# Optimization experiments

Hardware: AMD Instinct MI355X
Metric: run time of the kernel (lower is better)

Reference implementation:

```python
import jax, jax.numpy as jnp
import numpy as np


def _conv(x, w, b=None, stride=1, pad=0):
    y = jax.lax.conv_general_dilated(x, w, (stride, stride), [(pad, pad), (pad, pad)],
                                     dimension_numbers=('NCHW', 'OIHW', 'NCHW'))
    if b is not None:
        y = y + b[None, :, None, None]
    return y


def _slice3d(grid, guide):
    # Trilinear grid_sample, align_corners=False, zero padding.
    # grid: (N, C=12, D=8, GH, GW); guide: (N,1,H,W) in [-1,1]
    N, C, D, GH, GW = grid.shape
    H, W = guide.shape[2], guide.shape[3]
    xs = 2.0 * jnp.arange(W, dtype=grid.dtype) / max(W - 1, 1) - 1.0
    ys = 2.0 * jnp.arange(H, dtype=grid.dtype) / max(H - 1, 1) - 1.0
    gx = ((xs + 1.0) * GW - 1.0) * 0.5               # (W,)
    gy = ((ys + 1.0) * GH - 1.0) * 0.5               # (H,)
    gz = ((guide[:, 0] + 1.0) * D - 1.0) * 0.5       # (N,H,W)
    x0f = jnp.floor(gx); y0f = jnp.floor(gy); z0f = jnp.floor(gz)
    fx = gx - x0f; fy = gy - y0f; fz = gz - z0f
    x0 = x0f.astype(jnp.int32); y0 = y0f.astype(jnp.int32); z0 = z0f.astype(jnp.int32)
    gf = grid.reshape(N, C, D * GH * GW)

    def corner(zi, yi, xi, wz, wy, wx):
        mask = ((zi >= 0) & (zi < D)) & ((yi >= 0) & (yi < GH))[None, :, None] & ((xi >= 0) & (xi < GW))[None, None, :]
        zc = jnp.clip(zi, 0, D - 1); yc = jnp.clip(yi, 0, GH - 1); xc = jnp.clip(xi, 0, GW - 1)
        flat = zc * (GH * GW) + yc[None, :, None] * GW + xc[None, None, :]   # (N,H,W)
        v = jnp.take_along_axis(gf, flat.reshape(N, 1, H * W), axis=2).reshape(N, C, H, W)
        w = (wz * wy[None, :, None] * wx[None, None, :]) * mask.astype(grid.dtype)  # (N,H,W)
        return v * w[:, None]

    out = jnp.zeros((N, C, H, W), grid.dtype)
    for dz in (0, 1):
        for dy in (0, 1):
            for dx in (0, 1):
                out = out + corner(z0 + dz, y0 + dy, x0 + dx,
                                   fz if dz else 1.0 - fz,
                                   fy if dy else 1.0 - fy,
                                   fx if dx else 1.0 - fx)
    return out


def setup_inputs() -> dict:
    key = jax.random.key(0)
    ks = jax.random.split(key, 40)
    def w(i, shape):
        return jax.random.normal(ks[i], shape, jnp.float32) * 0.05
    return {
        'low_res': jax.random.uniform(ks[0], (4, 3, 256, 256), jnp.float32),
        'full_res': jax.random.uniform(ks[1], (4, 1, 1024, 1024), jnp.float32),
        'w0': w(2, (8, 3, 3, 3)), 'b0': w(3, (8,)),
        'w1': w(4, (16, 8, 3, 3)), 'b1': w(5, (16,)),
        'w2': w(6, (32, 16, 3, 3)), 'b2': w(7, (32,)),
        'w3': w(8, (64, 32, 3, 3)), 'b3': w(9, (64,)),
        'wl0': w(10, (64, 64, 3, 3)), 'bl0': w(11, (64,)),
        'wl1': w(12, (64, 64, 3, 3)),
        'wg1': w(13, (128, 64, 3, 3)), 'bg1': w(14, (128,)),
        'wg2': w(15, (256, 128, 3, 3)), 'bg2': w(16, (256,)),
        'wf1': w(17, (256, 448, 1, 1)), 'bf1': w(18, (256,)),
        'wf2': w(19, (128, 256, 1, 1)), 'bf2': w(20, (128,)),
        'wf3': w(21, (64, 128, 1, 1)), 'bf3': w(22, (64,)),
        'wlin': w(23, (96, 64, 1, 1)), 'blin': w(24, (96,)),
        'wgd1': w(25, (16, 1, 3, 3)), 'bgd1': w(26, (16,)),
        'wgd2': w(27, (1, 16, 1, 1)), 'bgd2': w(28, (1,)),
        'wau1': w(29, (16, 1, 1, 1)), 'bau1': w(30, (16,)),
        'wau2': w(31, (1, 16, 1, 1)), 'bau2': w(32, (1,)),
        'wav1': w(33, (16, 1, 1, 1)), 'bav1': w(34, (16,)),
        'wav2': w(35, (1, 16, 1, 1)), 'bav2': w(36, (1,)),
    }


def reference(low_res, full_res, w0, b0, w1, b1, w2, b2, w3, b3, wl0, bl0, wl1,
              wg1, bg1, wg2, bg2, wf1, bf1, wf2, bf2, wf3, bf3, wlin, blin,
              wgd1, bgd1, wgd2, bgd2, wau1, bau1, wau2, bau2, wav1, bav1, wav2, bav2):
    relu = jax.nn.relu
    N = low_res.shape[0]
    H, W = full_res.shape[2], full_res.shape[3]
    fake = jax.image.resize(low_res, (N, 3, H, W), 'bilinear')
    # splat stack: 4 stride-2 convs
    x = relu(_conv(low_res, w0, b0, 2, 1))
    x = relu(_conv(x, w1, b1, 2, 1))
    x = relu(_conv(x, w2, b2, 2, 1))
    splat = relu(_conv(x, w3, b3, 2, 1))                 # (N,64,16,16)
    local = _conv(relu(_conv(splat, wl0, bl0, 1, 1)), wl1, None, 1, 1)
    # global branch
    a0 = splat.mean(axis=(2, 3), keepdims=True)
    x1 = relu(_conv(splat, wg1, bg1, 2, 1))
    a1 = x1.mean(axis=(2, 3), keepdims=True)
    x2 = relu(_conv(x1, wg2, bg2, 2, 1))
    a2 = x2.mean(axis=(2, 3), keepdims=True)
    a = jnp.concatenate([a0, a1, a2], axis=1)            # (N,448,1,1)
    a = relu(_conv(a, wf1, bf1))
    a = relu(_conv(a, wf2, bf2))
    glob = relu(_conv(a, wf3, bf3))                      # (N,64,1,1)
    fused = relu(glob + local)
    fused = _conv(fused, wlin, blin)                     # (N,96,16,16)
    grid = fused.reshape(N, 12, 8, fused.shape[2], fused.shape[3])
    guidemap = jnp.tanh(_conv(relu(_conv(full_res, wgd1, bgd1, 1, 1)), wgd2, bgd2))
    coeff = _slice3d(grid, guidemap)                     # (N,12,H,W)
    Y = full_res * coeff[:, 3:4] + coeff[:, 0:3].sum(axis=1, keepdims=True)
    U0 = full_res * coeff[:, 7:8] + coeff[:, 4:7].sum(axis=1, keepdims=True)
    V0 = full_res * coeff[:, 11:12] + coeff[:, 8:11].sum(axis=1, keepdims=True)
    U = jnp.tanh(_conv(relu(_conv(U0, wau1, bau1)), wau2, bau2)) + fake[:, 1:2]
    V = jnp.tanh(_conv(relu(_conv(V0, wav1, bav1)), wav2, bav2)) + fake[:, 2:3]
    return jnp.concatenate([Y, U, V], axis=1)
```

## Files before the change

kernel.cpp:

```cpp
#include <hip/hip_runtime.h>
#include <math.h>


__device__ __forceinline__ float tanh_fast(float x) {
    float e = __expf(2.0f * x);
    return 1.0f - 2.0f / (e + 1.0f);
}

template<int CIN, int COUT, int HIN, int WIN, int HOUT, int WOUT>
__global__ __launch_bounds__(256) void conv_s2_small(
    const float* __restrict__ in, const float* __restrict__ w,
    const float* __restrict__ b, float* __restrict__ out)
{
    int idx = blockIdx.x * 256 + threadIdx.x;
    int wo = idx % WOUT; int t = idx / WOUT;
    int ho = t % HOUT; t /= HOUT;
    int co = t % COUT; int n = t / COUT;
    float acc = b[co];
    int hi0 = ho * 2 - 1, wi0 = wo * 2 - 1;
    const float* wp = w + (size_t)co * CIN * 9;
    #pragma unroll
    for (int ci = 0; ci < CIN; ++ci) {
        const float* ip = in + ((size_t)(n * CIN + ci)) * HIN * WIN;
        const float* wc = wp + ci * 9;
        #pragma unroll
        for (int kh = 0; kh < 3; ++kh) {
            int hi = hi0 + kh;
            if ((unsigned)hi >= (unsigned)HIN) continue;
            const float* row = ip + hi * WIN;
            #pragma unroll
            for (int kw = 0; kw < 3; ++kw) {
                int wi = wi0 + kw;
                if ((unsigned)wi >= (unsigned)WIN) continue;
                acc = fmaf(wc[kh * 3 + kw], row[wi], acc);
            }
        }
    }
    out[idx] = fmaxf(acc, 0.0f);
}

template<int CIN, int PARTS, int STRIDE, bool RELU, bool HASB,
         int COUT, int HIN, int WIN, int HOUT, int WOUT>
__device__ __forceinline__ void conv_p_dev(
    const float* __restrict__ in, const float* __restrict__ w,
    const float* __restrict__ b, float* __restrict__ out,
    int tb, float* red)
{
    constexpr int CPT = CIN / PARTS;
    constexpr int OPB = 256 / PARTS;
    int part = threadIdx.x / OPB;
    int oidx = threadIdx.x % OPB;
    int o = tb * OPB + oidx;
    int wo = o % WOUT; int t = o / WOUT;
    int ho = t % HOUT; t /= HOUT;
    int co = t % COUT; int n = t / COUT;
    int hi0 = ho * STRIDE - 1, wi0 = wo * STRIDE - 1;
    const float* wp = w + ((size_t)co * CIN + part * CPT) * 9;
    const float* ip = in + ((size_t)n * CIN + part * CPT) * HIN * WIN;
    float acc = 0.0f;
    #pragma unroll
    for (int ci = 0; ci < CPT; ++ci) {
        const float* ic = ip + (size_t)ci * HIN * WIN;
        const float* wc = wp + ci * 9;
        #pragma unroll
        for (int kh = 0; kh < 3; ++kh) {
            int hi = hi0 + kh;
            if ((unsigned)hi >= (unsigned)HIN) continue;
            const float* row = ic + hi * WIN;
            #pragma unroll
            for (int kw = 0; kw < 3; ++kw) {
                int wi = wi0 + kw;
                if ((unsigned)wi >= (unsigned)WIN) continue;
                acc = fmaf(wc[kh * 3 + kw], row[wi], acc);
            }
        }
    }
    red[threadIdx.x] = acc;
    __syncthreads();
    if (part == 0) {
        float s = acc;
        #pragma unroll
        for (int p = 1; p < PARTS; ++p) s += red[p * OPB + oidx];
        if (HASB) s += b[co];
        if (RELU) s = fmaxf(s, 0.0f);
        out[o] = s;
    }
}

__global__ __launch_bounds__(256) void conv2_k(
    const float* __restrict__ in, const float* __restrict__ w,
    const float* __restrict__ b, float* __restrict__ out)
{
    __shared__ float red[256];
    conv_p_dev<16, 4, 2, true, true, 32, 64, 64, 32, 32>(in, w, b, out, blockIdx.x, red);
}

__global__ __launch_bounds__(256) void conv3_k(
    const float* __restrict__ in, const float* __restrict__ w,
    const float* __restrict__ b, float* __restrict__ out)
{
    __shared__ float red[256];
    conv_p_dev<32, 8, 2, true, true, 64, 32, 32, 16, 16>(in, w, b, out, blockIdx.x, red);
}

__global__ __launch_bounds__(256) void k5_l0_g1_means(
    const float* __restrict__ splat,
    const float* __restrict__ wl0, const float* __restrict__ bl0, float* __restrict__ l0o,
    const float* __restrict__ wg1, const float* __restrict__ bg1, float* __restrict__ x1,
    float* __restrict__ avec)
{
    __shared__ float red[256];
    int bid = blockIdx.x;
    if (bid < 4096) {
        conv_p_dev<64, 16, 1, true, true, 64, 16, 16, 16, 16>(splat, wl0, bl0, l0o, bid, red);
    } else if (bid < 6144) {
        conv_p_dev<64, 16, 2, true, true, 128, 16, 16, 8, 8>(splat, wg1, bg1, x1, bid - 4096, red);
    } else {
        int wid = (bid - 6144) * 4 + (threadIdx.x >> 6);
        int lane = threadIdx.x & 63;
        int n = wid >> 6, c = wid & 63;
        const float* p = splat + ((size_t)(n * 64 + c)) * 256;
        float s = p[lane] + p[lane + 64] + p[lane + 128] + p[lane + 192];
        #pragma unroll
        for (int off = 32; off; off >>= 1) s += __shfl_down(s, off, 64);
        if (lane == 0) avec[n * 448 + c] = s * (1.0f / 256.0f);
    }
}

__global__ __launch_bounds__(256) void k6_l1_g2_means(
    const float* __restrict__ l0o, const float* __restrict__ wl1, float* __restrict__ localb,
    const float* __restrict__ x1, const float* __restrict__ wg2,
    const float* __restrict__ bg2, float* __restrict__ x2,
    float* __restrict__ avec)
{
    __shared__ float red[256];
    int bid = blockIdx.x;
    if (bid < 4096) {
        conv_p_dev<64, 16, 1, false, false, 64, 16, 16, 16, 16>(l0o, wl1, nullptr, localb, bid, red);
    } else if (bid < 5120) {
        conv_p_dev<128, 16, 2, true, true, 256, 8, 8, 4, 4>(x1, wg2, bg2, x2, bid - 4096, red);
    } else {
        int wid = (bid - 5120) * 4 + (threadIdx.x >> 6);
        int lane = threadIdx.x & 63;
        int n = wid >> 7, c = wid & 127;
        const float* p = x1 + ((size_t)(n * 128 + c)) * 64;
        float s = p[lane];
        #pragma unroll
        for (int off = 32; off; off >>= 1) s += __shfl_down(s, off, 64);
        if (lane == 0) avec[n * 448 + 64 + c] = s * (1.0f / 64.0f);
    }
}

__global__ __launch_bounds__(256) void kfc_fuse(
    const float* __restrict__ avec, const float* __restrict__ x2,
    const float* __restrict__ wf1, const float* __restrict__ bf1,
    const float* __restrict__ wf2, const float* __restrict__ bf2,
    const float* __restrict__ wf3, const float* __restrict__ bf3,
    const float* __restrict__ local,
    const float* __restrict__ wlin, const float* __restrict__ blin,
    float* __restrict__ grid)
{
    __shared__ float a[448];
    __shared__ float h1[256];
    __shared__ float h2[128];
    __shared__ float gl[64];
    int n = blockIdx.x / 96; int k = blockIdx.x % 96; int t = threadIdx.x;
    if (t < 192) a[t] = avec[n * 448 + t];
    {
        const float* p = x2 + ((size_t)(n * 256 + t)) * 16;
        float s = 0.0f;
        #pragma unroll
        for (int i = 0; i < 16; ++i) s += p[i];
        a[192 + t] = s * (1.0f / 16.0f);
    }
    __syncthreads();
    {
        float a0 = 0, a1 = 0, a2 = 0, a3 = 0;
        const float* wp = wf1 + (size_t)t * 448;
        for (int i = 0; i < 448; i += 4) {
            a0 = fmaf(wp[i], a[i], a0); a1 = fmaf(wp[i + 1], a[i + 1], a1);
            a2 = fmaf(wp[i + 2], a[i + 2], a2); a3 = fmaf(wp[i + 3], a[i + 3], a3);
        }
        h1[t] = fmaxf(a0 + a1 + a2 + a3 + bf1[t], 0.0f);
    }
    __syncthreads();
    if (t < 128) {
        float a0 = 0, a1 = 0, a2 = 0, a3 = 0;
        const float* wp = wf2 + (size_t)t * 256;
        for (int i = 0; i < 256; i += 4) {
            a0 = fmaf(wp[i], h1[i], a0); a1 = fmaf(wp[i + 1], h1[i + 1], a1);
            a2 = fmaf(wp[i + 2], h1[i + 2], a2); a3 = fmaf(wp[i + 3], h1[i + 3], a3);
        }
        h2[t] = fmaxf(a0 + a1 + a2 + a3 + bf2[t], 0.0f);
    }
    __syncthreads();
    if (t < 64) {
        float a0 = 0, a1 = 0, a2 = 0, a3 = 0;
        const float* wp = wf3 + (size_t)t * 128;
        for (int i = 0; i < 128; i += 4) {
            a0 = fmaf(wp[i], h2[i], a0); a1 = fmaf(wp[i + 1], h2[i + 1], a1);
            a2 = fmaf(wp[i + 2], h2[i + 2], a2); a3 = fmaf(wp[i + 3], h2[i + 3], a3);
        }
        gl[t] = fmaxf(a0 + a1 + a2 + a3 + bf3[t], 0.0f);
    }
    __syncthreads();
    float acc = blin[k];
    const float* wp = wlin + k * 64;
    const float* lo = local + (size_t)n * 64 * 256 + t;
    #pragma unroll 8
    for (int c = 0; c < 64; ++c)
        acc = fmaf(wp[c], fmaxf(gl[c] + lo[c * 256], 0.0f), acc);
    int ch = k >> 3; int z = k & 7;
    grid[(((size_t)(n * 8 + z)) * 256 + t) * 12 + ch] = acc;
}

__global__ __launch_bounds__(256) void hdr_out_v2(
    const float* __restrict__ full, const float* __restrict__ low,
    const float* __restrict__ grid,
    const float* __restrict__ wgd1, const float* __restrict__ bgd1,
    const float* __restrict__ wgd2, const float* __restrict__ bgd2,
    const float* __restrict__ wau1, const float* __restrict__ bau1,
    const float* __restrict__ wau2, const float* __restrict__ bau2,
    const float* __restrict__ wav1, const float* __restrict__ bav1,
    const float* __restrict__ wav2, const float* __restrict__ bav2,
    float* __restrict__ out)
{
    int tid = blockIdx.x * 256 + threadIdx.x;
    int x0 = (tid & 255) << 2;
    int y = (tid >> 8) & 1023;
    int n = tid >> 18;
    const float* fp = full + ((size_t)n << 20);

    float v[3][6];
    #pragma unroll
    for (int r = 0; r < 3; ++r) {
        int yy = y + r - 1;
        bool okr = (unsigned)yy < 1024u;
        const float* row = fp + (size_t)yy * 1024;
        if (okr) {
            float4 m = *(const float4*)(row + x0);
            v[r][1] = m.x; v[r][2] = m.y; v[r][3] = m.z; v[r][4] = m.w;
            v[r][0] = (x0 > 0) ? row[x0 - 1] : 0.0f;
            v[r][5] = (x0 < 1020) ? row[x0 + 4] : 0.0f;
        } else {
            #pragma unroll
            for (int j = 0; j < 6; ++j) v[r][j] = 0.0f;
        }
    }

    float gacc[4];
    float bb = bgd2[0];
    #pragma unroll
    for (int px = 0; px < 4; ++px) gacc[px] = bb;
    #pragma unroll
    for (int k = 0; k < 16; ++k) {
        const float* wk = wgd1 + k * 9;
        float q0 = wk[0], q1 = wk[1], q2 = wk[2];
        float q3 = wk[3], q4 = wk[4], q5 = wk[5];
        float q6 = wk[6], q7 = wk[7], q8 = wk[8];
        float bk = bgd1[k], wo = wgd2[k];
        #pragma unroll
        for (int px = 0; px < 4; ++px) {
            float h = bk;
            h = fmaf(q0, v[0][px], h); h = fmaf(q1, v[0][px + 1], h); h = fmaf(q2, v[0][px + 2], h);
            h = fmaf(q3, v[1][px], h); h = fmaf(q4, v[1][px + 1], h); h = fmaf(q5, v[1][px + 2], h);
            h = fmaf(q6, v[2][px], h); h = fmaf(q7, v[2][px + 1], h); h = fmaf(q8, v[2][px + 2], h);
            gacc[px] = fmaf(wo, fmaxf(h, 0.0f), gacc[px]);
        }
    }

    const float* gbase = grid + (size_t)n * 24576;
    float Yo[4], Uo[4], Vo[4];

    #pragma unroll
    for (int px = 0; px < 4; ++px) {
        int x = x0 + px;
        float g = tanh_fast(gacc[px]);

        float gxc = (x * (32.0f / 1023.0f) - 1.0f) * 0.5f;
        float gyc = (y * (32.0f / 1023.0f) - 1.0f) * 0.5f;
        float gzc = 4.0f * g + 3.5f;
        float x0f = floorf(gxc), y0f = floorf(gyc), z0f = floorf(gzc);
        float fx = gxc - x0f, fy = gyc - y0f, fz = gzc - z0f;
        int ix = (int)x0f, iy = (int)y0f, iz = (int)z0f;

        float wx0 = (ix >= 0 && ix < 16) ? (1.0f - fx) : 0.0f;
        float wx1 = (ix + 1 < 16) ? fx : 0.0f;
        float wy0 = (iy >= 0 && iy < 16) ? (1.0f - fy) : 0.0f;
        float wy1 = (iy + 1 < 16) ? fy : 0.0f;
        float wz0 = (iz >= 0 && iz < 8) ? (1.0f - fz) : 0.0f;
        float wz1 = (iz + 1 >= 0 && iz + 1 < 8) ? fz : 0.0f;
        int xi0 = min(max(ix, 0), 15), xi1 = min(ix + 1, 15);
        int yi0 = min(max(iy, 0), 15), yi1 = min(iy + 1, 15);
        int zi0 = min(max(iz, 0), 7),  zi1 = min(max(iz + 1, 0), 7);

        float w00 = wy0 * wx0, w01 = wy0 * wx1, w10 = wy1 * wx0, w11 = wy1 * wx1;
        int o00 = yi0 * 16 + xi0, o01 = yi0 * 16 + xi1;
        int o10 = yi1 * 16 + xi0, o11 = yi1 * 16 + xi1;
        int z0b = zi0 * 256, z1b = zi1 * 256;

        float acc[12];
        #pragma unroll
        for (int i = 0; i < 12; ++i) acc[i] = 0.0f;

        #define CORNER(OFF, WK) { \
            const float4* q = (const float4*)(gbase + (size_t)(OFF) * 12); \
            float wk_ = (WK); \
            float4 A = q[0], B = q[1], C = q[2]; \
            acc[0] = fmaf(wk_, A.x, acc[0]); acc[1] = fmaf(wk_, A.y, acc[1]); \
            acc[2] = fmaf(wk_, A.z, acc[2]); acc[3] = fmaf(wk_, A.w, acc[3]); \
            acc[4] = fmaf(wk_, B.x, acc[4]); acc[5] = fmaf(wk_, B.y, acc[5]); \
            acc[6] = fmaf(wk_, B.z, acc[6]); acc[7] = fmaf(wk_, B.w, acc[7]); \
            acc[8] = fmaf(wk_, C.x, acc[8]); acc[9] = fmaf(wk_, C.y, acc[9]); \
            acc[10] = fmaf(wk_, C.z, acc[10]); acc[11] = fmaf(wk_, C.w, acc[11]); }

        CORNER(z0b + o00, wz0 * w00)
        CORNER(z0b + o01, wz0 * w01)
        CORNER(z0b + o10, wz0 * w10)
        CORNER(z0b + o11, wz0 * w11)
        CORNER(z1b + o00, wz1 * w00)
        CORNER(z1b + o01, wz1 * w01)
        CORNER(z1b + o10, wz1 * w10)
        CORNER(z1b + o11, wz1 * w11)
        #undef CORNER

        float p = v[1][px + 1];
        float Yv = fmaf(p, acc[3],  acc[0] + acc[1] + acc[2]);
        float U0 = fmaf(p, acc[7],  acc[4] + acc[5] + acc[6]);
        float V0 = fmaf(p, acc[11], acc[8] + acc[9] + acc[10]);

        float uacc = bau2[0];
        #pragma unroll
        for (int k = 0; k < 16; ++k)
            uacc = fmaf(wau2[k], fmaxf(fmaf(wau1[k], U0, bau1[k]), 0.0f), uacc);
        float vacc = bav2[0];
        #pragma unroll
        for (int k = 0; k < 16; ++k)
            vacc = fmaf(wav2[k], fmaxf(fmaf(wav1[k], V0, bav1[k]), 0.0f), vacc);

        float sx = (x + 0.5f) * 0.25f - 0.5f;
        float sy = (y + 0.5f) * 0.25f - 0.5f;
        float sxf = floorf(sx), syf = floorf(sy);
        float fxl = sx - sxf, fyl = sy - syf;
        int jx0 = max((int)sxf, 0), jx1 = min((int)sxf + 1, 255);
        int jy0 = max((int)syf, 0), jy1 = min((int)syf + 1, 255);
        const float* lr1 = low + ((size_t)(n * 3 + 1)) * 65536;
        const float* lr2 = low + ((size_t)(n * 3 + 2)) * 65536;
        float f1 = (1.0f - fyl) * ((1.0f - fxl) * lr1[jy0 * 256 + jx0] + fxl * lr1[jy0 * 256 + jx1])
                 + fyl * ((1.0f - fxl) * lr1[jy1 * 256 + jx0] + fxl * lr1[jy1 * 256 + jx1]);
        float f2 = (1.0f - fyl) * ((1.0f - fxl) * lr2[jy0 * 256 + jx0] + fxl * lr2[jy0 * 256 + jx1])
                 + fyl * ((1.0f - fxl) * lr2[jy1 * 256 + jx0] + fxl * lr2[jy1 * 256 + jx1]);

        Yo[px] = Yv;
        Uo[px] = tanh_fast(uacc) + f1;
        Vo[px] = tanh_fast(vacc) + f2;
    }

    size_t base = ((size_t)n * 3) * 1048576 + (size_t)y * 1024 + x0;
    *(float4*)(out + base)            = make_float4(Yo[0], Yo[1], Yo[2], Yo[3]);
    *(float4*)(out + base + 1048576)  = make_float4(Uo[0], Uo[1], Uo[2], Uo[3]);
    *(float4*)(out + base + 2097152)  = make_float4(Vo[0], Vo[1], Vo[2], Vo[3]);
}

extern "C" void kernel_launch(void* const* d_in, const int* in_sizes, int n_in,
                              void* d_out, int out_size, void* d_ws, size_t ws_size,
                              hipStream_t stream)
{
    const float* low  = (const float*)d_in[0];
    const float* full = (const float*)d_in[1];
    const float* w0 = (const float*)d_in[2];  const float* b0 = (const float*)d_in[3];
    const float* w1 = (const float*)d_in[4];  const float* b1 = (const float*)d_in[5];
    const float* w2 = (const float*)d_in[6];  const float* b2 = (const float*)d_in[7];
    const float* w3 = (const float*)d_in[8];  const float* b3 = (const float*)d_in[9];
    const float* wl0 = (const float*)d_in[10]; const float* bl0 = (const float*)d_in[11];
    const float* wl1 = (const float*)d_in[12];
    const float* wg1 = (const float*)d_in[13]; const float* bg1 = (const float*)d_in[14];
    const float* wg2 = (const float*)d_in[15]; const float* bg2 = (const float*)d_in[16];
    const float* wf1 = (const float*)d_in[17]; const float* bf1 = (const float*)d_in[18];
    const float* wf2 = (const float*)d_in[19]; const float* bf2 = (const float*)d_in[20];
    const float* wf3 = (const float*)d_in[21]; const float* bf3 = (const float*)d_in[22];
    const float* wlin = (const float*)d_in[23]; const float* blin = (const float*)d_in[24];
    const float* wgd1 = (const float*)d_in[25]; const float* bgd1 = (const float*)d_in[26];
    const float* wgd2 = (const float*)d_in[27]; const float* bgd2 = (const float*)d_in[28];
    const float* wau1 = (const float*)d_in[29]; const float* bau1 = (const float*)d_in[30];
    const float* wau2 = (const float*)d_in[31]; const float* bau2 = (const float*)d_in[32];
    const float* wav1 = (const float*)d_in[33]; const float* bav1 = (const float*)d_in[34];
    const float* wav2 = (const float*)d_in[35]; const float* bav2 = (const float*)d_in[36];
    float* out = (float*)d_out;

    float* ws = (float*)d_ws;
    float* t0b    = ws;
    float* t1b    = t0b + 524288;
    float* t2b    = t1b + 262144;
    float* splat  = t2b + 131072;
    float* l0o    = splat + 65536;
    float* localb = l0o + 65536;
    float* x1b    = localb + 65536;
    float* x2b    = x1b + 32768;
    float* avec   = x2b + 16384;
    float* gridb  = avec + 1792;

    conv_s2_small<3, 8, 256, 256, 128, 128><<<2048, 256, 0, stream>>>(low, w0, b0, t0b);
    conv_s2_small<8, 16, 128, 128, 64, 64><<<1024, 256, 0, stream>>>(t0b, w1, b1, t1b);
    conv2_k<<<2048, 256, 0, stream>>>(t1b, w2, b2, t2b);
    conv3_k<<<2048, 256, 0, stream>>>(t2b, w3, b3, splat);
    k5_l0_g1_means<<<6208, 256, 0, stream>>>(splat, wl0, bl0, l0o, wg1, bg1, x1b, avec);
    k6_l1_g2_means<<<5248, 256, 0, stream>>>(l0o, wl1, localb, x1b, wg2, bg2, x2b, avec);
    kfc_fuse<<<384, 256, 0, stream>>>(avec, x2b, wf1, bf1, wf2, bf2, wf3, bf3,
                                      localb, wlin, blin, gridb);
    hdr_out_v2<<<4096, 256, 0, stream>>>(full, low, gridb,
        wgd1, bgd1, wgd2, bgd2, wau1, bau1, wau2, bau2, wav1, bav1, wav2, bav2, out);
}
```

Measured before the change: 362.7 us.

## Fuse all stages into one persistent kernel with hierarchical grid barriers

Replaces eight separate kernel launches with a single persistent kernel of 512 blocks. The blocks loop over each stage's work and synchronize through a two-level atomic grid barrier in workspace, which is cleared with a memset before launch. The aim is to remove launch overhead and the gaps between the many small early stages. In exchange, the large final per-pixel stage now runs on a fixed grid of 512 blocks with grid-stride loops. The barrier relies on all blocks being co-resident and includes a spin guard that could silently break ordering if it expires.

```diff
diff --git a/kernel.cpp b/kernel.cpp
--- a/kernel.cpp
+++ b/kernel.cpp
@@ -1,18 +1,45 @@
 #include <hip/hip_runtime.h>
 #include <math.h>
 
+
+#define NBLK 512
+#define NTHR 256
+#define GSZ (NBLK * NTHR)
 
 __device__ __forceinline__ float tanh_fast(float x) {
     float e = __expf(2.0f * x);
     return 1.0f - 2.0f / (e + 1.0f);
 }
 
+__device__ __forceinline__ void gsync(int* bar, int id) {
+    __syncthreads();
+    if (threadIdx.x == 0) {
+        int* base = bar + id * 1088;
+        int* grp  = base + ((blockIdx.x >> 4) << 5);
+        int* root = base + 1024;
+        int* flag = base + 1056;
+        __threadfence();
+        if (atomicAdd(grp, 1) == 15) {
+            if (atomicAdd(root, 1) == 31) {
+                __threadfence();
+                __hip_atomic_store(flag, 1, __ATOMIC_RELEASE, __HIP_MEMORY_SCOPE_AGENT);
+            }
+        }
+        int guard = 1 << 20;
+        while (__hip_atomic_load(flag, __ATOMIC_RELAXED, __HIP_MEMORY_SCOPE_AGENT) == 0
+               && --guard) {
+            __builtin_amdgcn_s_sleep(8);
+        }
+        __threadfence();
+    }
+    __syncthreads();
+}
+
 template<int CIN, int COUT, int HIN, int WIN, int HOUT, int WOUT>
-__global__ __launch_bounds__(256) void conv_s2_small(
+__device__ __forceinline__ void conv_s2_dev(
     const float* __restrict__ in, const float* __restrict__ w,
-    const float* __restrict__ b, float* __restrict__ out)
+    const float* __restrict__ b, float* __restrict__ out, int idx)
 {
-    int idx = blockIdx.x * 256 + threadIdx.x;
     int wo = idx % WOUT; int t = idx / WOUT;
     int ho = t % HOUT; t /= HOUT;
     int co = t % COUT; int n = t / COUT;
@@ -85,281 +112,294 @@
         if (RELU) s = fmaxf(s, 0.0f);
         out[o] = s;
     }
-}
-
-__global__ __launch_bounds__(256) void conv2_k(
-    const float* __restrict__ in, const float* __restrict__ w,
-    const float* __restrict__ b, float* __restrict__ out)
-{
-    __shared__ float red[256];
-    conv_p_dev<16, 4, 2, true, true, 32, 64, 64, 32, 32>(in, w, b, out, blockIdx.x, red);
-}
-
-__global__ __launch_bounds__(256) void conv3_k(
-    const float* __restrict__ in, const float* __restrict__ w,
-    const float* __restrict__ b, float* __restrict__ out)
-{
-    __shared__ float red[256];
-    conv_p_dev<32, 8, 2, true, true, 64, 32, 32, 16, 16>(in, w, b, out, blockIdx.x, red);
-}
-
-__global__ __launch_bounds__(256) void k5_l0_g1_means(
-    const float* __restrict__ splat,
-    const float* __restrict__ wl0, const float* __restrict__ bl0, float* __restrict__ l0o,
-    const float* __restrict__ wg1, const float* __restrict__ bg1, float* __restrict__ x1,
-    float* __restrict__ avec)
-{
-    __shared__ float red[256];
-    int bid = blockIdx.x;
-    if (bid < 4096) {
-        conv_p_dev<64, 16, 1, true, true, 64, 16, 16, 16, 16>(splat, wl0, bl0, l0o, bid, red);
-    } else if (bid < 6144) {
-        conv_p_dev<64, 16, 2, true, true, 128, 16, 16, 8, 8>(splat, wg1, bg1, x1, bid - 4096, red);
-    } else {
-        int wid = (bid - 6144) * 4 + (threadIdx.x >> 6);
-        int lane = threadIdx.x & 63;
-        int n = wid >> 6, c = wid & 63;
-        const float* p = splat + ((size_t)(n * 64 + c)) * 256;
-        float s = p[lane] + p[lane + 64] + p[lane + 128] + p[lane + 192];
-        #pragma unroll
-        for (int off = 32; off; off >>= 1) s += __shfl_down(s, off, 64);
-        if (lane == 0) avec[n * 448 + c] = s * (1.0f / 256.0f);
-    }
-}
-
-__global__ __launch_bounds__(256) void k6_l1_g2_means(
-    const float* __restrict__ l0o, const float* __restrict__ wl1, float* __restrict__ localb,
-    const float* __restrict__ x1, const float* __restrict__ wg2,
-    const float* __restrict__ bg2, float* __restrict__ x2,
-    float* __restrict__ avec)
-{
-    __shared__ float red[256];
-    int bid = blockIdx.x;
-    if (bid < 4096) {
-        conv_p_dev<64, 16, 1, false, false, 64, 16, 16, 16, 16>(l0o, wl1, nullptr, localb, bid, red);
-    } else if (bid < 5120) {
-        conv_p_dev<128, 16, 2, true, true, 256, 8, 8, 4, 4>(x1, wg2, bg2, x2, bid - 4096, red);
-    } else {
-        int wid = (bid - 5120) * 4 + (threadIdx.x >> 6);
-        int lane = threadIdx.x & 63;
-        int n = wid >> 7, c = wid & 127;
-        const float* p = x1 + ((size_t)(n * 128 + c)) * 64;
-        float s = p[lane];
-        #pragma unroll
-        for (int off = 32; off; off >>= 1) s += __shfl_down(s, off, 64);
-        if (lane == 0) avec[n * 448 + 64 + c] = s * (1.0f / 64.0f);
-    }
-}
-
-__global__ __launch_bounds__(256) void kfc_fuse(
-    const float* __restrict__ avec, const float* __restrict__ x2,
+    __syncthreads();
+}
+
+__global__ __launch_bounds__(256, 2) void hdrnet_mega2(
+    const float* __restrict__ low, const float* __restrict__ full,
+    const float* __restrict__ w0, const float* __restrict__ b0,
+    const float* __restrict__ w1, const float* __restrict__ b1,
+    const float* __restrict__ w2, const float* __restrict__ b2,
+    const float* __restrict__ w3, const float* __restrict__ b3,
+    const float* __restrict__ wl0, const float* __restrict__ bl0,
+    const float* __restrict__ wl1,
+    const float* __restrict__ wg1, const float* __restrict__ bg1,
+    const float* __restrict__ wg2, const float* __restrict__ bg2,
     const float* __restrict__ wf1, const float* __restrict__ bf1,
     const float* __restrict__ wf2, const float* __restrict__ bf2,
     const float* __restrict__ wf3, const float* __restrict__ bf3,
-    const float* __restrict__ local,
     const float* __restrict__ wlin, const float* __restrict__ blin,
-    float* __restrict__ grid)
-{
-    __shared__ float a[448];
-    __shared__ float h1[256];
-    __shared__ float h2[128];
-    __shared__ float gl[64];
-    int n = blockIdx.x / 96; int k = blockIdx.x % 96; int t = threadIdx.x;
-    if (t < 192) a[t] = avec[n * 448 + t];
-    {
-        const float* p = x2 + ((size_t)(n * 256 + t)) * 16;
-        float s = 0.0f;
-        #pragma unroll
-        for (int i = 0; i < 16; ++i) s += p[i];
-        a[192 + t] = s * (1.0f / 16.0f);
-    }
-    __syncthreads();
-    {
-        float a0 = 0, a1 = 0, a2 = 0, a3 = 0;
-        const float* wp = wf1 + (size_t)t * 448;
-        for (int i = 0; i < 448; i += 4) {
-            a0 = fmaf(wp[i], a[i], a0); a1 = fmaf(wp[i + 1], a[i + 1], a1);
-            a2 = fmaf(wp[i + 2], a[i + 2], a2); a3 = fmaf(wp[i + 3], a[i + 3], a3);
-        }
-        h1[t] = fmaxf(a0 + a1 + a2 + a3 + bf1[t], 0.0f);
-    }
-    __syncthreads();
-    if (t < 128) {
-        float a0 = 0, a1 = 0, a2 = 0, a3 = 0;
-        const float* wp = wf2 + (size_t)t * 256;
-        for (int i = 0; i < 256; i += 4) {
-            a0 = fmaf(wp[i], h1[i], a0); a1 = fmaf(wp[i + 1], h1[i + 1], a1);
-            a2 = fmaf(wp[i + 2], h1[i + 2], a2); a3 = fmaf(wp[i + 3], h1[i + 3], a3);
-        }
-        h2[t] = fmaxf(a0 + a1 + a2 + a3 + bf2[t], 0.0f);
-    }
-    __syncthreads();
-    if (t < 64) {
-        float a0 = 0, a1 = 0, a2 = 0, a3 = 0;
-        const float* wp = wf3 + (size_t)t * 128;
-        for (int i = 0; i < 128; i += 4) {
-            a0 = fmaf(wp[i], h2[i], a0); a1 = fmaf(wp[i + 1], h2[i + 1], a1);
-            a2 = fmaf(wp[i + 2], h2[i + 2], a2); a3 = fmaf(wp[i + 3], h2[i + 3], a3);
-        }
-        gl[t] = fmaxf(a0 + a1 + a2 + a3 + bf3[t], 0.0f);
-    }
-    __syncthreads();
-    float acc = blin[k];
-    const float* wp = wlin + k * 64;
-    const float* lo = local + (size_t)n * 64 * 256 + t;
-    #pragma unroll 8
-    for (int c = 0; c < 64; ++c)
-        acc = fmaf(wp[c], fmaxf(gl[c] + lo[c * 256], 0.0f), acc);
-    int ch = k >> 3; int z = k & 7;
-    grid[(((size_t)(n * 8 + z)) * 256 + t) * 12 + ch] = acc;
-}
-
-__global__ __launch_bounds__(256) void hdr_out_v2(
-    const float* __restrict__ full, const float* __restrict__ low,
-    const float* __restrict__ grid,
     const float* __restrict__ wgd1, const float* __restrict__ bgd1,
     const float* __restrict__ wgd2, const float* __restrict__ bgd2,
     const float* __restrict__ wau1, const float* __restrict__ bau1,
     const float* __restrict__ wau2, const float* __restrict__ bau2,
     const float* __restrict__ wav1, const float* __restrict__ bav1,
     const float* __restrict__ wav2, const float* __restrict__ bav2,
-    float* __restrict__ out)
+    float* __restrict__ out, int* __restrict__ bar, float* __restrict__ wsf)
 {
-    int tid = blockIdx.x * 256 + threadIdx.x;
-    int x0 = (tid & 255) << 2;
-    int y = (tid >> 8) & 1023;
-    int n = tid >> 18;
-    const float* fp = full + ((size_t)n << 20);
-
-    float v[3][6];
-    #pragma unroll
-    for (int r = 0; r < 3; ++r) {
-        int yy = y + r - 1;
-        bool okr = (unsigned)yy < 1024u;
-        const float* row = fp + (size_t)yy * 1024;
-        if (okr) {
-            float4 m = *(const float4*)(row + x0);
-            v[r][1] = m.x; v[r][2] = m.y; v[r][3] = m.z; v[r][4] = m.w;
-            v[r][0] = (x0 > 0) ? row[x0 - 1] : 0.0f;
-            v[r][5] = (x0 < 1020) ? row[x0 + 4] : 0.0f;
+    __shared__ float smem[896];
+    float* red = smem;
+    const int bid = blockIdx.x;
+    const int tid = bid * NTHR + threadIdx.x;
+
+    float* t0b    = wsf;
+    float* t1b    = t0b + 524288;
+    float* t2b    = t1b + 262144;
+    float* splat  = t2b + 131072;
+    float* l0o    = splat + 65536;
+    float* localb = l0o + 65536;
+    float* x1b    = localb + 65536;
+    float* x2b    = x1b + 32768;
+    float* avec   = x2b + 16384;
+    float* gridb  = avec + 1792;
+
+    for (int idx = tid; idx < 524288; idx += GSZ)
+        conv_s2_dev<3, 8, 256, 256, 128, 128>(low, w0, b0, t0b, idx);
+    gsync(bar, 0);
+
+    for (int idx = tid; idx < 262144; idx += GSZ)
+        conv_s2_dev<8, 16, 128, 128, 64, 64>(t0b, w1, b1, t1b, idx);
+    gsync(bar, 1);
+
+    for (int tb = bid; tb < 2048; tb += NBLK)
+        conv_p_dev<16, 4, 2, true, true, 32, 64, 64, 32, 32>(t1b, w2, b2, t2b, tb, red);
+    gsync(bar, 2);
+
+    for (int tb = bid; tb < 2048; tb += NBLK)
+        conv_p_dev<32, 8, 2, true, true, 64, 32, 32, 16, 16>(t2b, w3, b3, splat, tb, red);
+    gsync(bar, 3);
+
+    for (int tb = bid; tb < 6144; tb += NBLK) {
+        if (tb < 4096)
+            conv_p_dev<64, 16, 1, true, true, 64, 16, 16, 16, 16>(splat, wl0, bl0, l0o, tb, red);
+        else
+            conv_p_dev<64, 16, 2, true, true, 128, 16, 16, 8, 8>(splat, wg1, bg1, x1b, tb - 4096, red);
+    }
+    gsync(bar, 4);
+
+    for (int tb = bid; tb < 5312; tb += NBLK) {
+        if (tb < 4096) {
+            conv_p_dev<64, 16, 1, false, false, 64, 16, 16, 16, 16>(l0o, wl1, nullptr, localb, tb, red);
+        } else if (tb < 5120) {
+            conv_p_dev<128, 16, 2, true, true, 256, 8, 8, 4, 4>(x1b, wg2, bg2, x2b, tb - 4096, red);
         } else {
-            #pragma unroll
-            for (int j = 0; j < 6; ++j) v[r][j] = 0.0f;
-        }
-    }
-
-    float gacc[4];
-    float bb = bgd2[0];
-    #pragma unroll
-    for (int px = 0; px < 4; ++px) gacc[px] = bb;
-    #pragma unroll
-    for (int k = 0; k < 16; ++k) {
-        const float* wk = wgd1 + k * 9;
-        float q0 = wk[0], q1 = wk[1], q2 = wk[2];
-        float q3 = wk[3], q4 = wk[4], q5 = wk[5];
-        float q6 = wk[6], q7 = wk[7], q8 = wk[8];
-        float bk = bgd1[k], wo = wgd2[k];
+            int wid = (tb - 5120) * 4 + (threadIdx.x >> 6);
+            int lane = threadIdx.x & 63;
+            if (wid < 256) {
+                int n = wid >> 6, c = wid & 63;
+                const float* p = splat + ((size_t)(n * 64 + c)) * 256;
+                float s = p[lane] + p[lane + 64] + p[lane + 128] + p[lane + 192];
+                #pragma unroll
+                for (int off = 32; off; off >>= 1) s += __shfl_down(s, off, 64);
+                if (lane == 0) avec[n * 448 + c] = s * (1.0f / 256.0f);
+            } else {
+                int w2id = wid - 256;
+                int n = w2id >> 7, c = w2id & 127;
+                const float* p = x1b + ((size_t)(n * 128 + c)) * 64;
+                float s = p[lane];
+                #pragma unroll
+                for (int off = 32; off; off >>= 1) s += __shfl_down(s, off, 64);
+                if (lane == 0) avec[n * 448 + 64 + c] = s * (1.0f / 64.0f);
+            }
+            __syncthreads();
+        }
+    }
+    gsync(bar, 5);
+
+    if (bid < 384) {
+        float* a   = smem;
+        float* h1  = smem + 448;
+        float* h2  = smem + 704;
+        float* gl  = smem + 832;
+        int n = bid / 96; int k = bid % 96; int t = threadIdx.x;
+        if (t < 192) a[t] = avec[n * 448 + t];
+        {
+            const float* p = x2b + ((size_t)(n * 256 + t)) * 16;
+            float s = 0.0f;
+            #pragma unroll
+            for (int i = 0; i < 16; ++i) s += p[i];
+            a[192 + t] = s * (1.0f / 16.0f);
+        }
+        __syncthreads();
+        {
+            float a0 = 0, a1 = 0, a2 = 0, a3 = 0;
+            const float* wp = wf1 + (size_t)t * 448;
+            for (int i = 0; i < 448; i += 4) {
+                a0 = fmaf(wp[i], a[i], a0); a1 = fmaf(wp[i + 1], a[i + 1], a1);
+                a2 = fmaf(wp[i + 2], a[i + 2], a2); a3 = fmaf(wp[i + 3], a[i + 3], a3);
+            }
+            float s = a0 + a1 + a2 + a3 + bf1[t];
+            __syncthreads();
+            h1[t] = fmaxf(s, 0.0f);
+        }
+        __syncthreads();
+        if (t < 128) {
+            float a0 = 0, a1 = 0, a2 = 0, a3 = 0;
+            const float* wp = wf2 + (size_t)t * 256;
+            for (int i = 0; i < 256; i += 4) {
+                a0 = fmaf(wp[i], h1[i], a0); a1 = fmaf(wp[i + 1], h1[i + 1], a1);
+                a2 = fmaf(wp[i + 2], h1[i + 2], a2); a3 = fmaf(wp[i + 3], h1[i + 3], a3);
+            }
+            h2[t] = fmaxf(a0 + a1 + a2 + a3 + bf2[t], 0.0f);
+        }
+        __syncthreads();
+        if (t < 64) {
+            float a0 = 0, a1 = 0, a2 = 0, a3 = 0;
+            const float* wp = wf3 + (size_t)t * 128;
+            for (int i = 0; i < 128; i += 4) {
+                a0 = fmaf(wp[i], h2[i], a0); a1 = fmaf(wp[i + 1], h2[i + 1], a1);
+                a2 = fmaf(wp[i + 2], h2[i + 2], a2); a3 = fmaf(wp[i + 3], h2[i + 3], a3);
+            }
+            gl[t] = fmaxf(a0 + a1 + a2 + a3 + bf3[t], 0.0f);
+        }
+        __syncthreads();
+        float acc = blin[k];
+        const float* wp = wlin + k * 64;
+        const float* lo = localb + (size_t)n * 64 * 256 + t;
+        #pragma unroll 8
+        for (int c = 0; c < 64; ++c)
+            acc = fmaf(wp[c], fmaxf(gl[c] + lo[c * 256], 0.0f), acc);
+        int ch = k >> 3; int z = k & 7;
+        gridb[(((size_t)(n * 8 + z)) * 256 + t) * 12 + ch] = acc;
+    }
+    gsync(bar, 6);
+
+    for (int task = tid; task < 1048576; task += GSZ) {
+        int x0 = (task & 255) << 2;
+        int y = (task >> 8) & 1023;
+        int n = task >> 18;
+        const float* fp = full + ((size_t)n << 20);
+
+        float v[3][6];
+        #pragma unroll
+        for (int r = 0; r < 3; ++r) {
+            int yy = y + r - 1;
+            bool okr = (unsigned)yy < 1024u;
+            const float* row = fp + (size_t)yy * 1024;
+            if (okr) {
+                float4 m = *(const float4*)(row + x0);
+                v[r][1] = m.x; v[r][2] = m.y; v[r][3] = m.z; v[r][4] = m.w;
+                v[r][0] = (x0 > 0) ? row[x0 - 1] : 0.0f;
+                v[r][5] = (x0 < 1020) ? row[x0 + 4] : 0.0f;
+            } else {
+                #pragma unroll
+                for (int j = 0; j < 6; ++j) v[r][j] = 0.0f;
+            }
+        }
+
+        float gacc[4];
+        float bb = bgd2[0];
+        #pragma unroll
+        for (int px = 0; px < 4; ++px) gacc[px] = bb;
+        #pragma unroll
+        for (int k = 0; k < 16; ++k) {
+            const float* wk = wgd1 + k * 9;
+            float q0 = wk[0], q1 = wk[1], q2 = wk[2];
+            float q3 = wk[3], q4 = wk[4], q5 = wk[5];
+            float q6 = wk[6], q7 = wk[7], q8 = wk[8];
+            float bk = bgd1[k], wo = wgd2[k];
+            #pragma unroll
+            for (int px = 0; px < 4; ++px) {
+                float h = bk;
+                h = fmaf(q0, v[0][px], h); h = fmaf(q1, v[0][px + 1], h); h = fmaf(q2, v[0][px + 2], h);
+                h = fmaf(q3, v[1][px], h); h = fmaf(q4, v[1][px + 1], h); h = fmaf(q5, v[1][px + 2], h);
+                h = fmaf(q6, v[2][px], h); h = fmaf(q7, v[2][px + 1], h); h = fmaf(q8, v[2][px + 2], h);
+                gacc[px] = fmaf(wo, fmaxf(h, 0.0f), gacc[px]);
+            }
+        }
+
+        const float* gbase = gridb + (size_t)n * 24576;
+        float Yo[4], Uo[4], Vo[4];
+
         #pragma unroll
         for (int px = 0; px < 4; ++px) {
-            float h = bk;
-            h = fmaf(q0, v[0][px], h); h = fmaf(q1, v[0][px + 1], h); h = fmaf(q2, v[0][px + 2], h);
-            h = fmaf(q3, v[1][px], h); h = fmaf(q4, v[1][px + 1], h); h = fmaf(q5, v[1][px + 2], h);
-            h = fmaf(q6, v[2][px], h); h = fmaf(q7, v[2][px + 1], h); h = fmaf(q8, v[2][px + 2], h);
-            gacc[px] = fmaf(wo, fmaxf(h, 0.0f), gacc[px]);
-        }
-    }
-
-    const float* gbase = grid + (size_t)n * 24576;
-    float Yo[4], Uo[4], Vo[4];
-
-    #pragma unroll
-    for (int px = 0; px < 4; ++px) {
-        int x = x0 + px;
-        float g = tanh_fast(gacc[px]);
-
-        float gxc = (x * (32.0f / 1023.0f) - 1.0f) * 0.5f;
-        float gyc = (y * (32.0f / 1023.0f) - 1.0f) * 0.5f;
-        float gzc = 4.0f * g + 3.5f;
-        float x0f = floorf(gxc), y0f = floorf(gyc), z0f = floorf(gzc);
-        float fx = gxc - x0f, fy = gyc - y0f, fz = gzc - z0f;
-        int ix = (int)x0f, iy = (int)y0f, iz = (int)z0f;
-
-        float wx0 = (ix >= 0 && ix < 16) ? (1.0f - fx) : 0.0f;
-        float wx1 = (ix + 1 < 16) ? fx : 0.0f;
-        float wy0 = (iy >= 0 && iy < 16) ? (1.0f - fy) : 0.0f;
-        float wy1 = (iy + 1 < 16) ? fy : 0.0f;
-        float wz0 = (iz >= 0 && iz < 8) ? (1.0f - fz) : 0.0f;
-        float wz1 = (iz + 1 >= 0 && iz + 1 < 8) ? fz : 0.0f;
-        int xi0 = min(max(ix, 0), 15), xi1 = min(ix + 1, 15);
-        int yi0 = min(max(iy, 0), 15), yi1 = min(iy + 1, 15);
-        int zi0 = min(max(iz, 0), 7),  zi1 = min(max(iz + 1, 0), 7);
-
-        float w00 = wy0 * wx0, w01 = wy0 * wx1, w10 = wy1 * wx0, w11 = wy1 * wx1;
-        int o00 = yi0 * 16 + xi0, o01 = yi0 * 16 + xi1;
-        int o10 = yi1 * 16 + xi0, o11 = yi1 * 16 + xi1;
-        int z0b = zi0 * 256, z1b = zi1 * 256;
-
-        float acc[12];
-        #pragma unroll
-        for (int i = 0; i < 12; ++i) acc[i] = 0.0f;
-
-        #define CORNER(OFF, WK) { \
-            const float4* q = (const float4*)(gbase + (size_t)(OFF) * 12); \
-            float wk_ = (WK); \
-            float4 A = q[0], B = q[1], C = q[2]; \
-            acc[0] = fmaf(wk_, A.x, acc[0]); acc[1] = fmaf(wk_, A.y, acc[1]); \
-            acc[2] = fmaf(wk_, A.z, acc[2]); acc[3] = fmaf(wk_, A.w, acc[3]); \
-            acc[4] = fmaf(wk_, B.x, acc[4]); acc[5] = fmaf(wk_, B.y, acc[5]); \
-            acc[6] = fmaf(wk_, B.z, acc[6]); acc[7] = fmaf(wk_, B.w, acc[7]); \
-            acc[8] = fmaf(wk_, C.x, acc[8]); acc[9] = fmaf(wk_, C.y, acc[9]); \
-            acc[10] = fmaf(wk_, C.z, acc[10]); acc[11] = fmaf(wk_, C.w, acc[11]); }
-
-        CORNER(z0b + o00, wz0 * w00)
-        CORNER(z0b + o01, wz0 * w01)
-        CORNER(z0b + o10, wz0 * w10)
-        CORNER(z0b + o11, wz0 * w11)
-        CORNER(z1b + o00, wz1 * w00)
-        CORNER(z1b + o01, wz1 * w01)
-        CORNER(z1b + o10, wz1 * w10)
-        CORNER(z1b + o11, wz1 * w11)
-        #undef CORNER
-
-        float p = v[1][px + 1];
-        float Yv = fmaf(p, acc[3],  acc[0] + acc[1] + acc[2]);
-        float U0 = fmaf(p, acc[7],  acc[4] + acc[5] + acc[6]);
-        float V0 = fmaf(p, acc[11], acc[8] + acc[9] + acc[10]);
-
-        float uacc = bau2[0];
-        #pragma unroll
-        for (int k = 0; k < 16; ++k)
-            uacc = fmaf(wau2[k], fmaxf(fmaf(wau1[k], U0, bau1[k]), 0.0f), uacc);
-        float vacc = bav2[0];
-        #pragma unroll
-        for (int k = 0; k < 16; ++k)
-            vacc = fmaf(wav2[k], fmaxf(fmaf(wav1[k], V0, bav1[k]), 0.0f), vacc);
-
-        float sx = (x + 0.5f) * 0.25f - 0.5f;
-        float sy = (y + 0.5f) * 0.25f - 0.5f;
-        float sxf = floorf(sx), syf = floorf(sy);
-        float fxl = sx - sxf, fyl = sy - syf;
-        int jx0 = max((int)sxf, 0), jx1 = min((int)sxf + 1, 255);
-        int jy0 = max((int)syf, 0), jy1 = min((int)syf + 1, 255);
-        const float* lr1 = low + ((size_t)(n * 3 + 1)) * 65536;
-        const float* lr2 = low + ((size_t)(n * 3 + 2)) * 65536;
-        float f1 = (1.0f - fyl) * ((1.0f - fxl) * lr1[jy0 * 256 + jx0] + fxl * lr1[jy0 * 256 + jx1])
-                 + fyl * ((1.0f - fxl) * lr1[jy1 * 256 + jx0] + fxl * lr1[jy1 * 256 + jx1]);
-        float f2 = (1.0f - fyl) * ((1.0f - fxl) * lr2[jy0 * 256 + jx0] + fxl * lr2[jy0 * 256 + jx1])
-                 + fyl * ((1.0f - fxl) * lr2[jy1 * 256 + jx0] + fxl * lr2[jy1 * 256 + jx1]);
-
-        Yo[px] = Yv;
-        Uo[px] = tanh_fast(uacc) + f1;
-        Vo[px] = tanh_fast(vacc) + f2;
-    }
-
-    size_t base = ((size_t)n * 3) * 1048576 + (size_t)y * 1024 + x0;
-    *(float4*)(out + base)            = make_float4(Yo[0], Yo[1], Yo[2], Yo[3]);
-    *(float4*)(out + base + 1048576)  = make_float4(Uo[0], Uo[1], Uo[2], Uo[3]);
-    *(float4*)(out + base + 2097152)  = make_float4(Vo[0], Vo[1], Vo[2], Vo[3]);
+            int x = x0 + px;
+            float g = tanh_fast(gacc[px]);
+
+            float gxc = (x * (32.0f / 1023.0f) - 1.0f) * 0.5f;
+            float gyc = (y * (32.0f / 1023.0f) - 1.0f) * 0.5f;
+            float gzc = 4.0f * g + 3.5f;
+            float x0f = floorf(gxc), y0f = floorf(gyc), z0f = floorf(gzc);
+            float fx = gxc - x0f, fy = gyc - y0f, fz = gzc - z0f;
+            int ix = (int)x0f, iy = (int)y0f, iz = (int)z0f;
+
+            float wx0 = (ix >= 0 && ix < 16) ? (1.0f - fx) : 0.0f;
+            float wx1 = (ix + 1 < 16) ? fx : 0.0f;
+            float wy0 = (iy >= 0 && iy < 16) ? (1.0f - fy) : 0.0f;
+            float wy1 = (iy + 1 < 16) ? fy : 0.0f;
+            float wz0 = (iz >= 0 && iz < 8) ? (1.0f - fz) : 0.0f;
+            float wz1 = (iz + 1 >= 0 && iz + 1 < 8) ? fz : 0.0f;
+            int xi0 = min(max(ix, 0), 15), xi1 = min(ix + 1, 15);
+            int yi0 = min(max(iy, 0), 15), yi1 = min(iy + 1, 15);
+            int zi0 = min(max(iz, 0), 7),  zi1 = min(max(iz + 1, 0), 7);
+
+            float w00 = wy0 * wx0, w01 = wy0 * wx1, w10 = wy1 * wx0, w11 = wy1 * wx1;
+            int o00 = yi0 * 16 + xi0, o01 = yi0 * 16 + xi1;
+            int o10 = yi1 * 16 + xi0, o11 = yi1 * 16 + xi1;
+            int z0b = zi0 * 256, z1b = zi1 * 256;
+
+            float acc[12];
+            #pragma unroll
+            for (int i = 0; i < 12; ++i) acc[i] = 0.0f;
+
+            #define CORNER(OFF, WK) { \
+                const float4* q = (const float4*)(gbase + (size_t)(OFF) * 12); \
+                float wk_ = (WK); \
+                float4 A = q[0], B = q[1], C = q[2]; \
+                acc[0] = fmaf(wk_, A.x, acc[0]); acc[1] = fmaf(wk_, A.y, acc[1]); \
+                acc[2] = fmaf(wk_, A.z, acc[2]); acc[3] = fmaf(wk_, A.w, acc[3]); \
+                acc[4] = fmaf(wk_, B.x, acc[4]); acc[5] = fmaf(wk_, B.y, acc[5]); \
+                acc[6] = fmaf(wk_, B.z, acc[6]); acc[7] = fmaf(wk_, B.w, acc[7]); \
+                acc[8] = fmaf(wk_, C.x, acc[8]); acc[9] = fmaf(wk_, C.y, acc[9]); \
+                acc[10] = fmaf(wk_, C.z, acc[10]); acc[11] = fmaf(wk_, C.w, acc[11]); }
+
+            CORNER(z0b + o00, wz0 * w00)
+            CORNER(z0b + o01, wz0 * w01)
+            CORNER(z0b + o10, wz0 * w10)
+            CORNER(z0b + o11, wz0 * w11)
+            CORNER(z1b + o00, wz1 * w00)
+            CORNER(z1b + o01, wz1 * w01)
+            CORNER(z1b + o10, wz1 * w10)
+            CORNER(z1b + o11, wz1 * w11)
+            #undef CORNER
+
+            float p = v[1][px + 1];
+            float Yv = fmaf(p, acc[3],  acc[0] + acc[1] + acc[2]);
+            float U0 = fmaf(p, acc[7],  acc[4] + acc[5] + acc[6]);
+            float V0 = fmaf(p, acc[11], acc[8] + acc[9] + acc[10]);
+
+            float uacc = bau2[0];
+            #pragma unroll
+            for (int k = 0; k < 16; ++k)
+                uacc = fmaf(wau2[k], fmaxf(fmaf(wau1[k], U0, bau1[k]), 0.0f), uacc);
+            float vacc = bav2[0];
+            #pragma unroll
+            for (int k = 0; k < 16; ++k)
+                vacc = fmaf(wav2[k], fmaxf(fmaf(wav1[k], V0, bav1[k]), 0.0f), vacc);
+
+            float sx = (x + 0.5f) * 0.25f - 0.5f;
+            float sy = (y + 0.5f) * 0.25f - 0.5f;
+            float sxf = floorf(sx), syf = floorf(sy);
+            float fxl = sx - sxf, fyl = sy - syf;
+            int jx0 = max((int)sxf, 0), jx1 = min((int)sxf + 1, 255);
+            int jy0 = max((int)syf, 0), jy1 = min((int)syf + 1, 255);
+            const float* lr1 = low + ((size_t)(n * 3 + 1)) * 65536;
+            const float* lr2 = low + ((size_t)(n * 3 + 2)) * 65536;
+            float f1 = (1.0f - fyl) * ((1.0f - fxl) * lr1[jy0 * 256 + jx0] + fxl * lr1[jy0 * 256 + jx1])
+                     + fyl * ((1.0f - fxl) * lr1[jy1 * 256 + jx0] + fxl * lr1[jy1 * 256 + jx1]);
+            float f2 = (1.0f - fyl) * ((1.0f - fxl) * lr2[jy0 * 256 + jx0] + fxl * lr2[jy0 * 256 + jx1])
+                     + fyl * ((1.0f - fxl) * lr2[jy1 * 256 + jx0] + fxl * lr2[jy1 * 256 + jx1]);
+
+            Yo[px] = Yv;
+            Uo[px] = tanh_fast(uacc) + f1;
+            Vo[px] = tanh_fast(vacc) + f2;
+        }
+
+        size_t base = ((size_t)n * 3) * 1048576 + (size_t)y * 1024 + x0;
+        *(float4*)(out + base)            = make_float4(Yo[0], Yo[1], Yo[2], Yo[3]);
+        *(float4*)(out + base + 1048576)  = make_float4(Uo[0], Uo[1], Uo[2], Uo[3]);
+        *(float4*)(out + base + 2097152)  = make_float4(Vo[0], Vo[1], Vo[2], Vo[3]);
+    }
 }
 
 extern "C" void kernel_launch(void* const* d_in, const int* in_sizes, int n_in,
@@ -388,26 +428,13 @@
     const float* wav2 = (const float*)d_in[35]; const float* bav2 = (const float*)d_in[36];
     float* out = (float*)d_out;
 
-    float* ws = (float*)d_ws;
-    float* t0b    = ws;
-    float* t1b    = t0b + 524288;
-    float* t2b    = t1b + 262144;
-    float* splat  = t2b + 131072;
-    float* l0o    = splat + 65536;
-    float* localb = l0o + 65536;
-    float* x1b    = localb + 65536;
-    float* x2b    = x1b + 32768;
-    float* avec   = x2b + 16384;
-    float* gridb  = avec + 1792;
-
-    conv_s2_small<3, 8, 256, 256, 128, 128><<<2048, 256, 0, stream>>>(low, w0, b0, t0b);
-    conv_s2_small<8, 16, 128, 128, 64, 64><<<1024, 256, 0, stream>>>(t0b, w1, b1, t1b);
-    conv2_k<<<2048, 256, 0, stream>>>(t1b, w2, b2, t2b);
-    conv3_k<<<2048, 256, 0, stream>>>(t2b, w3, b3, splat);
-    k5_l0_g1_means<<<6208, 256, 0, stream>>>(splat, wl0, bl0, l0o, wg1, bg1, x1b, avec);
-    k6_l1_g2_means<<<5248, 256, 0, stream>>>(l0o, wl1, localb, x1b, wg2, bg2, x2b, avec);
-    kfc_fuse<<<384, 256, 0, stream>>>(avec, x2b, wf1, bf1, wf2, bf2, wf3, bf3,
-                                      localb, wlin, blin, gridb);
-    hdr_out_v2<<<4096, 256, 0, stream>>>(full, low, gridb,
-        wgd1, bgd1, wgd2, bgd2, wau1, bau1, wau2, bau2, wav1, bav1, wav2, bav2, out);
-}
+    int* bar = (int*)d_ws;
+    float* wsf = (float*)d_ws + 8192;
+
+    hipMemsetAsync(bar, 0, 8192 * sizeof(int), stream);
+    hdrnet_mega2<<<NBLK, NTHR, 0, stream>>>(
+        low, full, w0, b0, w1, b1, w2, b2, w3, b3, wl0, bl0, wl1,
+        wg1, bg1, wg2, bg2, wf1, bf1, wf2, bf2, wf3, bf3, wlin, blin,
+        wgd1, bgd1, wgd2, bgd2, wau1, bau1, wau2, bau2, wav1, bav1, wav2, bav2,
+        out, bar, wsf);
+}
```

Result: slower. 576.0 us (+58.8%).
